# Optimization experiments

Hardware: AMD Instinct MI355X
Metric: run time of the kernel (lower is better)

The kernel has to match this reference:

```python
import jax, jax.numpy as jnp
import numpy as np

H, B, S, E, V, C = 1024, 1024, 128, 6, 3, 10


def setup_inputs() -> dict:
    key = jax.random.key(0)
    ks = jax.random.split(key, 18)
    sH = 1.0 / np.sqrt(H)

    def n(k, shape, scale):
        return (jax.random.normal(k, shape, dtype=jnp.float32) * scale)

    return {
        'x': jax.random.randint(ks[0], (B, S), 0, V),
        'emb': n(ks[1], (V, E), 1.0),
        'W_gx': n(ks[2], (H, E), 1.0 / np.sqrt(E)),
        'W_gh': n(ks[3], (H, H), sH),
        'b_g': n(ks[4], (H, 1), sH),
        'W_ix': n(ks[5], (H, E), 1.0 / np.sqrt(E)),
        'W_ih': n(ks[6], (H, H), sH),
        'b_i': n(ks[7], (H, 1), sH),
        'W_fx': n(ks[8], (H, E), 1.0 / np.sqrt(E)),
        'W_fh': n(ks[9], (H, H), sH),
        'b_f': n(ks[10], (H, 1), sH),
        'W_ox': n(ks[11], (H, E), 1.0 / np.sqrt(E)),
        'W_oh': n(ks[12], (H, H), sH),
        'b_o': n(ks[13], (H, 1), sH),
        'W_ph': n(ks[14], (C, H), sH),
        'b_p': n(ks[15], (C, 1), sH),
        'h_init': n(ks[16], (H, B), 1.0),
        'c_init': n(ks[17], (H, B), 1.0),
    }


def reference(x, emb, W_gx, W_gh, b_g, W_ix, W_ih, b_i, W_fx, W_fh, b_f,
              W_ox, W_oh, b_o, W_ph, b_p, h_init, c_init):
    T = x.shape[1] - 1  # torch loop runs over seq_length - 1 steps
    e = emb[x[:, :T]]  # [B, T, E]
    # Precompute all input-to-gate projections in one batched contraction each.
    Xg = jnp.einsum('he,bte->thb', W_gx, e)  # [T, H, B]
    Xi = jnp.einsum('he,bte->thb', W_ix, e)
    Xf = jnp.einsum('he,bte->thb', W_fx, e)
    Xo = jnp.einsum('he,bte->thb', W_ox, e)

    def step(carry, xs):
        h, c = carry  # [H, B]
        xg, xi, xf, xo = xs
        g = jnp.tanh(xg + W_gh @ h + b_g)
        i = jax.nn.sigmoid(xi + W_ih @ h + b_i)
        f = jax.nn.sigmoid(xf + W_fh @ h + b_f)
        o = jax.nn.sigmoid(xo + W_oh @ h + b_o)
        c2 = g * i + c * f
        h2 = jnp.tanh(c2) * o
        return (h2, c2), None

    (h, c), _ = jax.lax.scan(step, (h_init, c_init), (Xg, Xi, Xf, Xo))
    p = W_ph @ h + b_p  # [C, B]
    return jax.nn.log_softmax(p.T, axis=-1)  # [B, C]
```

## Files before the change

kernel.cpp:

```cpp
#include <hip/hip_runtime.h>

constexpr int kH = 1024;
constexpr int kB = 1024;
constexpr int kS = 128;
constexpr int kT = 127;
constexpr int kE = 6;
constexpr int kV = 3;
constexpr int kC = 10;

typedef short s16x8 __attribute__((ext_vector_type(8)));
typedef short s16x4 __attribute__((ext_vector_type(4)));
typedef float f32x4 __attribute__((ext_vector_type(4)));
typedef unsigned short u16;

__device__ __forceinline__ float b2f(u16 u) {
    return __uint_as_float(((unsigned)u) << 16);
}
__device__ __forceinline__ u16 f2b(float f) {
    unsigned u = __float_as_uint(f);
    return (u16)((u + 0x7FFFu + ((u >> 16) & 1u)) >> 16);
}
__device__ __forceinline__ float sigmoid_fast(float x) {
    return 1.0f / (1.0f + __expf(-x));
}
__device__ __forceinline__ float tanh_fast(float x) {
    return 2.0f / (1.0f + __expf(-2.0f * x)) - 1.0f;
}
__device__ __forceinline__ float clamp30(float x) {
    return fminf(fmaxf(x, -30.0f), 30.0f);
}

__device__ __forceinline__ void async_copy16(const u16* g, u16* l) {
    __builtin_amdgcn_global_load_lds(
        (const __attribute__((address_space(1))) void*)g,
        (__attribute__((address_space(3))) void*)l, 16, 0, 0);
}

__global__ __launch_bounds__(256) void prep_weights(
    const float* __restrict__ Wgh, const float* __restrict__ Wih,
    const float* __restrict__ Wfh, const float* __restrict__ Woh,
    u16* __restrict__ wsw)
{
    unsigned grp = blockIdx.x * 256 + threadIdx.x;
    const int lane = grp & 63;
    const int lm   = lane & 15;
    const int quad = lane >> 4;
    const int k0   = (grp >> 6) & 7;
    const int g    = (grp >> 9) & 3;
    const int kc   = (grp >> 11) & 3;
    const int by   = grp >> 13;
    const float* src = (g == 0) ? Wgh : (g == 1) ? Wih : (g == 2) ? Wfh : Woh;
    const int row = by * 16 + lm;
    const int k   = kc * 256 + k0 * 32 + quad * 8;
    f32x4 v0 = *(const f32x4*)(src + (size_t)row * kH + k);
    f32x4 v1 = *(const f32x4*)(src + (size_t)row * kH + k + 4);
    s16x8 o;
#pragma unroll
    for (int j = 0; j < 4; ++j) o[j] = (short)f2b(v0[j]);
#pragma unroll
    for (int j = 0; j < 4; ++j) o[4 + j] = (short)f2b(v1[j]);
    *(s16x8*)(wsw + (size_t)grp * 8) = o;
}

__global__ __launch_bounds__(1024) void prep_hc(
    const float* __restrict__ h0, const float* __restrict__ c0,
    u16* __restrict__ hA, float* __restrict__ cT)
{
    __shared__ float th[32][33];
    __shared__ float tc[32][33];
    int b = blockIdx.x * 32 + threadIdx.x;
    int h = blockIdx.y * 32 + threadIdx.y;
    th[threadIdx.y][threadIdx.x] = h0[(size_t)h * kB + b];
    tc[threadIdx.y][threadIdx.x] = c0[(size_t)h * kB + b];
    __syncthreads();
    int ob = blockIdx.x * 32 + threadIdx.y;
    int oh = blockIdx.y * 32 + threadIdx.x;
    hA[(size_t)ob * kH + oh] = f2b(th[threadIdx.x][threadIdx.y]);
    cT[(size_t)ob * kH + oh] = tc[threadIdx.x][threadIdx.y];
}

__global__ __launch_bounds__(256) void prep_q(
    const float* __restrict__ Wgx, const float* __restrict__ Wix,
    const float* __restrict__ Wfx, const float* __restrict__ Wox,
    const float* __restrict__ bg,  const float* __restrict__ bi,
    const float* __restrict__ bf_, const float* __restrict__ bo,
    const float* __restrict__ emb, float* __restrict__ Qp)
{
    int tid = blockIdx.x * blockDim.x + threadIdx.x;
    if (tid >= 4096) return;
    int g   = tid >> 10;
    int hr4 = (tid & 1023) >> 2;
    int v   = tid & 3;
    const float* Wx = (g == 0) ? Wgx : (g == 1) ? Wix : (g == 2) ? Wfx : Wox;
    const float* bb = (g == 0) ? bg  : (g == 1) ? bi  : (g == 2) ? bf_ : bo;
    f32x4 o;
#pragma unroll
    for (int reg = 0; reg < 4; ++reg) {
        int row = hr4 * 4 + reg;
        float s = bb[row];
        if (v < kV) {
#pragma unroll
            for (int e = 0; e < kE; ++e) s += Wx[row * kE + e] * emb[v * kE + e];
        }
        o[reg] = s;
    }
    *(f32x4*)(Qp + (size_t)tid * 4) = o;
}

__global__ __launch_bounds__(256, 2) void lstm_step(
    const u16* __restrict__ wsw, const float* __restrict__ Qp,
    const int* __restrict__ x, int t,
    const short* __restrict__ hin, u16* __restrict__ hout,
    float* __restrict__ cT)
{
    __shared__ u16 wlds[2][16384];

    const int tid  = threadIdx.x;
    const int lane = tid & 63;
    const int wave = tid >> 6;
    const int lm   = lane & 15;
    const int quad = lane >> 4;
    const int blk  = blockIdx.x;
    const int xcd  = blk & 7;
    const int slot = blk >> 3;
    const int by   = xcd * 8 + (slot & 7);
    const int bx   = slot >> 3;
    const int r0 = by * 16;
    const int c0 = bx * 128 + wave * 32;

    const u16* wswblk = wsw + (size_t)by * 65536;

#pragma unroll
    for (int rr = 0; rr < 8; ++rr) {
        const int ub = wave * 4096 + rr * 512;
        async_copy16(wswblk + ub + lane * 8, &wlds[0][ub]);
    }

    int vv[2];
#pragma unroll
    for (int nt = 0; nt < 2; ++nt) {
        int v = x[(size_t)(c0 + nt * 16 + lm) * kS + t];
        vv[nt] = (v < 0) ? 0 : (v > kV - 1) ? (kV - 1) : v;
    }
    f32x4 qv[2][4];
#pragma unroll
    for (int nt = 0; nt < 2; ++nt)
#pragma unroll
        for (int g = 0; g < 4; ++g)
            qv[nt][g] = *(const f32x4*)(Qp +
                (size_t)(((g * 256 + by * 4 + quad) * 4 + vv[nt]) * 4));
    f32x4 cold[2];
#pragma unroll
    for (int nt = 0; nt < 2; ++nt)
        cold[nt] = *(const f32x4*)(cT +
            (size_t)(c0 + nt * 16 + lm) * kH + r0 + quad * 4);

    const int koff = quad * 8;
    const short* hrow0 = hin + (size_t)(c0 + lm) * kH + koff;
    const short* hrow1 = hin + (size_t)(c0 + 16 + lm) * kH + koff;
    s16x8 br[6][2];
#pragma unroll
    for (int s = 0; s < 5; ++s) {
        br[s][0] = *(const s16x8*)(hrow0 + s * 32);
        br[s][1] = *(const s16x8*)(hrow1 + s * 32);
    }

    f32x4 acc[4][2];
    const f32x4 zero = {0.f, 0.f, 0.f, 0.f};
#pragma unroll
    for (int g = 0; g < 4; ++g)
#pragma unroll
        for (int n = 0; n < 2; ++n) acc[g][n] = zero;

    asm volatile("s_waitcnt vmcnt(0)" ::: "memory");
    __syncthreads();

#pragma unroll
    for (int k0 = 0; k0 < 32; ++k0) {
        if ((k0 & 7) == 0 && k0 > 0) {
            asm volatile("s_waitcnt vmcnt(0)" ::: "memory");
            __syncthreads();
        }
        if ((k0 & 7) == 0 && k0 < 24) {
            const int nc = (k0 >> 3) + 1;
            const u16* gsrc = wswblk + (size_t)nc * 16384;
#pragma unroll
            for (int rr = 0; rr < 8; ++rr) {
                const int ub = wave * 4096 + rr * 512;
                async_copy16(gsrc + ub + lane * 8, &wlds[nc & 1][ub]);
            }
        }
        if (k0 + 5 < 32) {
            const int s = (k0 + 5) % 6;
            br[s][0] = *(const s16x8*)(hrow0 + (k0 + 5) * 32);
            br[s][1] = *(const s16x8*)(hrow1 + (k0 + 5) * 32);
        }
        const int cur = k0 % 6;
        const int buf = (k0 >> 3) & 1;
#pragma unroll
        for (int g = 0; g < 4; ++g) {
            const int f = ((g * 8 + (k0 & 7)) * 64 + lane) * 8;
            s16x8 a = *(const s16x8*)&wlds[buf][f];
            acc[g][0] = __builtin_amdgcn_mfma_f32_16x16x32_bf16(a, br[cur][0], acc[g][0], 0, 0, 0);
            acc[g][1] = __builtin_amdgcn_mfma_f32_16x16x32_bf16(a, br[cur][1], acc[g][1], 0, 0, 0);
        }
    }

#pragma unroll
    for (int nt = 0; nt < 2; ++nt) {
        const int c = c0 + nt * 16 + lm;
        const int rb = r0 + quad * 4;
        f32x4 cnew;
        s16x4 hnew;
#pragma unroll
        for (int reg = 0; reg < 4; ++reg) {
            float pg = clamp30(acc[0][nt][reg] + qv[nt][0][reg]);
            float pi = clamp30(acc[1][nt][reg] + qv[nt][1][reg]);
            float pf = clamp30(acc[2][nt][reg] + qv[nt][2][reg]);
            float po = clamp30(acc[3][nt][reg] + qv[nt][3][reg]);
            float gg = tanh_fast(pg);
            float ii = sigmoid_fast(pi);
            float ff = sigmoid_fast(pf);
            float oo = sigmoid_fast(po);
            float c2 = gg * ii + cold[nt][reg] * ff;
            c2 = fminf(fmaxf(c2, -200.0f), 200.0f);
            cnew[reg] = c2;
            hnew[reg] = (short)f2b(tanh_fast(c2) * oo);
        }
        *(f32x4*)(cT + (size_t)c * kH + rb) = cnew;
        *(s16x4*)(hout + (size_t)c * kH + rb) = hnew;
    }
}

__global__ __launch_bounds__(256) void logits_kernel(
    const u16* __restrict__ hT, const float* __restrict__ Wph,
    const float* __restrict__ bp, float* __restrict__ out)
{
    const int wave = threadIdx.x >> 6;
    const int lane = threadIdx.x & 63;
    const int b = blockIdx.x * 4 + wave;

    const u16* hp = hT + (size_t)b * kH + lane * 16;
    float hf[16];
#pragma unroll
    for (int j = 0; j < 16; ++j) hf[j] = b2f(hp[j]);

    float p[kC];
#pragma unroll
    for (int cls = 0; cls < kC; ++cls) {
        const float* wp = Wph + (size_t)cls * kH + lane * 16;
        float s = 0.f;
#pragma unroll
        for (int j = 0; j < 16; ++j) s += hf[j] * wp[j];
#pragma unroll
        for (int off = 1; off < 64; off <<= 1) s += __shfl_xor(s, off, 64);
        p[cls] = fminf(fmaxf(s + bp[cls], -1.0e4f), 1.0e4f);
    }

    float m = p[0];
#pragma unroll
    for (int cls = 1; cls < kC; ++cls) m = fmaxf(m, p[cls]);
    float se = 0.f;
#pragma unroll
    for (int cls = 0; cls < kC; ++cls) se += __expf(p[cls] - m);
    float l = m + __logf(se);

    if (lane < kC) {
        float myp = p[0];
#pragma unroll
        for (int cls = 1; cls < kC; ++cls)
            if (lane == cls) myp = p[cls];
        out[(size_t)b * kC + lane] = myp - l;
    }
}

extern "C" void kernel_launch(void* const* d_in, const int* in_sizes, int n_in,
                              void* d_out, int out_size, void* d_ws, size_t ws_size,
                              hipStream_t stream)
{
    const int*   x   = (const int*)  d_in[0];
    const float* emb = (const float*)d_in[1];
    const float* Wgx = (const float*)d_in[2];
    const float* Wgh = (const float*)d_in[3];
    const float* bg  = (const float*)d_in[4];
    const float* Wix = (const float*)d_in[5];
    const float* Wih = (const float*)d_in[6];
    const float* bi  = (const float*)d_in[7];
    const float* Wfx = (const float*)d_in[8];
    const float* Wfh = (const float*)d_in[9];
    const float* bf_ = (const float*)d_in[10];
    const float* Wox = (const float*)d_in[11];
    const float* Woh = (const float*)d_in[12];
    const float* bo  = (const float*)d_in[13];
    const float* Wph = (const float*)d_in[14];
    const float* bp  = (const float*)d_in[15];
    const float* h0  = (const float*)d_in[16];
    const float* c0  = (const float*)d_in[17];

    char* ws = (char*)d_ws;
    float* Qp  = (float*)ws;
    u16*   hA  = (u16*)(ws + (64 << 10));
    u16*   hB  = hA + (size_t)kB * kH;
    float* cT  = (float*)(hB + (size_t)kB * kH);
    u16*   wsw = (u16*)(cT + (size_t)kB * kH);

    prep_weights<<<dim3(2048), dim3(256), 0, stream>>>(Wgh, Wih, Wfh, Woh, wsw);
    prep_hc<<<dim3(kB / 32, kH / 32), dim3(32, 32), 0, stream>>>(h0, c0, hA, cT);
    prep_q<<<dim3(16), dim3(256), 0, stream>>>(Wgx, Wix, Wfx, Wox, bg, bi, bf_, bo, emb, Qp);

    for (int t = 0; t < kT; ++t) {
        const u16* hin  = (t & 1) ? hB : hA;
        u16*       hout = (t & 1) ? hA : hB;
        lstm_step<<<dim3(512), dim3(256), 0, stream>>>(
            wsw, Qp, x, t, (const short*)hin, hout, cT);
    }
    logits_kernel<<<dim3(kB / 4), dim3(256), 0, stream>>>(hB, Wph, bp, (float*)d_out);
}
```

Baseline: 2.932 ms.

## Widen per-wave batch tile to 64 and stream half the weights from global

Each block now covers 256 batch columns (64 per wave) instead of 128, so the grid halves to 256 blocks and every weight fragment feeds four MFMAs instead of two. Only the first half of the K range of weights is staged in LDS, loaded once with no double-buffer barriers, and the second half is read directly from global memory into registers with a small software prefetch pipeline. The aim is to cut weight traffic per FLOP and remove the in-loop syncs. The cost is much higher register pressure (launch_bounds min-blocks dropped) and only 256 blocks on a 256-CU part, one block per CU.

New measurement: 3.112 ms. 1.06x slower.

```diff
diff --git a/kernel.cpp b/kernel.cpp
--- a/kernel.cpp
+++ b/kernel.cpp
@@ -107,13 +107,13 @@
     *(f32x4*)(Qp + (size_t)tid * 4) = o;
 }
 
-__global__ __launch_bounds__(256, 2) void lstm_step(
+__global__ __launch_bounds__(256) void lstm_step(
     const u16* __restrict__ wsw, const float* __restrict__ Qp,
     const int* __restrict__ x, int t,
     const short* __restrict__ hin, u16* __restrict__ hout,
     float* __restrict__ cT)
 {
-    __shared__ u16 wlds[2][16384];
+    __shared__ u16 wl[32768];
 
     const int tid  = threadIdx.x;
     const int lane = tid & 63;
@@ -122,93 +122,98 @@
     const int quad = lane >> 4;
     const int blk  = blockIdx.x;
     const int xcd  = blk & 7;
-    const int slot = blk >> 3;
-    const int by   = xcd * 8 + (slot & 7);
-    const int bx   = slot >> 3;
+    const int s    = blk >> 3;
+    const int by   = xcd * 8 + (s & 7);
+    const int bx   = s >> 3;
     const int r0 = by * 16;
-    const int c0 = bx * 128 + wave * 32;
+    const int cw = bx * 256 + wave * 64;
 
     const u16* wswblk = wsw + (size_t)by * 65536;
 
 #pragma unroll
-    for (int rr = 0; rr < 8; ++rr) {
-        const int ub = wave * 4096 + rr * 512;
-        async_copy16(wswblk + ub + lane * 8, &wlds[0][ub]);
-    }
-
-    int vv[2];
-#pragma unroll
-    for (int nt = 0; nt < 2; ++nt) {
-        int v = x[(size_t)(c0 + nt * 16 + lm) * kS + t];
+    for (int rr = 0; rr < 16; ++rr) {
+        const int ub = wave * 8192 + rr * 512;
+        async_copy16(wswblk + ub + lane * 8, &wl[ub]);
+    }
+
+    int vv[4];
+#pragma unroll
+    for (int nt = 0; nt < 4; ++nt) {
+        int v = x[(size_t)(cw + nt * 16 + lm) * kS + t];
         vv[nt] = (v < 0) ? 0 : (v > kV - 1) ? (kV - 1) : v;
     }
-    f32x4 qv[2][4];
-#pragma unroll
-    for (int nt = 0; nt < 2; ++nt)
+    f32x4 qv[4][4];
+#pragma unroll
+    for (int nt = 0; nt < 4; ++nt)
 #pragma unroll
         for (int g = 0; g < 4; ++g)
             qv[nt][g] = *(const f32x4*)(Qp +
                 (size_t)(((g * 256 + by * 4 + quad) * 4 + vv[nt]) * 4));
-    f32x4 cold[2];
-#pragma unroll
-    for (int nt = 0; nt < 2; ++nt)
+    f32x4 cold[4];
+#pragma unroll
+    for (int nt = 0; nt < 4; ++nt)
         cold[nt] = *(const f32x4*)(cT +
-            (size_t)(c0 + nt * 16 + lm) * kH + r0 + quad * 4);
-
-    const int koff = quad * 8;
-    const short* hrow0 = hin + (size_t)(c0 + lm) * kH + koff;
-    const short* hrow1 = hin + (size_t)(c0 + 16 + lm) * kH + koff;
-    s16x8 br[6][2];
-#pragma unroll
-    for (int s = 0; s < 5; ++s) {
-        br[s][0] = *(const s16x8*)(hrow0 + s * 32);
-        br[s][1] = *(const s16x8*)(hrow1 + s * 32);
-    }
-
-    f32x4 acc[4][2];
-    const f32x4 zero = {0.f, 0.f, 0.f, 0.f};
-#pragma unroll
-    for (int g = 0; g < 4; ++g)
-#pragma unroll
-        for (int n = 0; n < 2; ++n) acc[g][n] = zero;
+            (size_t)(cw + nt * 16 + lm) * kH + r0 + quad * 4);
 
     asm volatile("s_waitcnt vmcnt(0)" ::: "memory");
     __syncthreads();
 
+    const int koff = quad * 8;
+    const short* hrow[4];
+#pragma unroll
+    for (int nt = 0; nt < 4; ++nt)
+        hrow[nt] = hin + (size_t)(cw + nt * 16 + lm) * kH + koff;
+
+    s16x8 ar[3][4];
+    s16x8 br[4][4];
+
+    auto loadA = [&](int k0, s16x8 d[4]) {
+        if (k0 < 16) {
+            const int base = ((k0 >> 3) * 4) * 4096 + (k0 & 7) * 512 + lane * 8;
+#pragma unroll
+            for (int g = 0; g < 4; ++g)
+                d[g] = *(const s16x8*)&wl[base + g * 4096];
+        } else {
+            const u16* gb = wswblk + ((size_t)(k0 >> 3) * 4) * 4096 +
+                            (size_t)(k0 & 7) * 512 + lane * 8;
+#pragma unroll
+            for (int g = 0; g < 4; ++g)
+                d[g] = *(const s16x8*)(gb + g * 4096);
+        }
+    };
+    auto loadB = [&](int k0, s16x8 d[4]) {
+#pragma unroll
+        for (int nt = 0; nt < 4; ++nt)
+            d[nt] = *(const s16x8*)(hrow[nt] + k0 * 32);
+    };
+
+    loadA(0, ar[0]); loadA(1, ar[1]);
+    loadB(0, br[0]); loadB(1, br[1]); loadB(2, br[2]);
+
+    f32x4 acc[4][4];
+    const f32x4 zero = {0.f, 0.f, 0.f, 0.f};
+#pragma unroll
+    for (int g = 0; g < 4; ++g)
+#pragma unroll
+        for (int nt = 0; nt < 4; ++nt) acc[g][nt] = zero;
+
 #pragma unroll
     for (int k0 = 0; k0 < 32; ++k0) {
-        if ((k0 & 7) == 0 && k0 > 0) {
-            asm volatile("s_waitcnt vmcnt(0)" ::: "memory");
-            __syncthreads();
-        }
-        if ((k0 & 7) == 0 && k0 < 24) {
-            const int nc = (k0 >> 3) + 1;
-            const u16* gsrc = wswblk + (size_t)nc * 16384;
-#pragma unroll
-            for (int rr = 0; rr < 8; ++rr) {
-                const int ub = wave * 4096 + rr * 512;
-                async_copy16(gsrc + ub + lane * 8, &wlds[nc & 1][ub]);
-            }
-        }
-        if (k0 + 5 < 32) {
-            const int s = (k0 + 5) % 6;
-            br[s][0] = *(const s16x8*)(hrow0 + (k0 + 5) * 32);
-            br[s][1] = *(const s16x8*)(hrow1 + (k0 + 5) * 32);
-        }
-        const int cur = k0 % 6;
-        const int buf = (k0 >> 3) & 1;
-#pragma unroll
-        for (int g = 0; g < 4; ++g) {
-            const int f = ((g * 8 + (k0 & 7)) * 64 + lane) * 8;
-            s16x8 a = *(const s16x8*)&wlds[buf][f];
-            acc[g][0] = __builtin_amdgcn_mfma_f32_16x16x32_bf16(a, br[cur][0], acc[g][0], 0, 0, 0);
-            acc[g][1] = __builtin_amdgcn_mfma_f32_16x16x32_bf16(a, br[cur][1], acc[g][1], 0, 0, 0);
-        }
-    }
-
-#pragma unroll
-    for (int nt = 0; nt < 2; ++nt) {
-        const int c = c0 + nt * 16 + lm;
+        if (k0 + 2 < 32) loadA(k0 + 2, ar[(k0 + 2) % 3]);
+        if (k0 + 3 < 32) loadB(k0 + 3, br[(k0 + 3) & 3]);
+        const s16x8* a = ar[k0 % 3];
+        const s16x8* b = br[k0 & 3];
+#pragma unroll
+        for (int g = 0; g < 4; ++g)
+#pragma unroll
+            for (int nt = 0; nt < 4; ++nt)
+                acc[g][nt] = __builtin_amdgcn_mfma_f32_16x16x32_bf16(
+                    a[g], b[nt], acc[g][nt], 0, 0, 0);
+    }
+
+#pragma unroll
+    for (int nt = 0; nt < 4; ++nt) {
+        const int c = cw + nt * 16 + lm;
         const int rb = r0 + quad * 4;
         f32x4 cnew;
         s16x4 hnew;
@@ -311,7 +316,7 @@
     for (int t = 0; t < kT; ++t) {
         const u16* hin  = (t & 1) ? hB : hA;
         u16*       hout = (t & 1) ? hA : hB;
-        lstm_step<<<dim3(512), dim3(256), 0, stream>>>(
+        lstm_step<<<dim3(256), dim3(256), 0, stream>>>(
             wsw, Qp, x, t, (const short*)hin, hout, cT);
     }
     logits_kernel<<<dim3(kB / 4), dim3(256), 0, stream>>>(hB, Wph, bp, (float*)d_out);
```
